# Performance work log

Measured on AMD Instinct MI355X. Metric: run time of the kernel, lower is better.

Reference implementation:

```python
import jax, jax.numpy as jnp
import numpy as np

D = 1024
H = 16
HD = D // H
EPS = 1e-5

def _layernorm(x, g, b):
    xf = x.astype(jnp.float32)
    mu = jnp.mean(xf, axis=-1, keepdims=True)
    var = jnp.mean(jnp.square(xf - mu), axis=-1, keepdims=True)
    return ((xf - mu) * jax.lax.rsqrt(var + EPS) * g + b).astype(x.dtype)

def setup_inputs() -> dict:
    key = jax.random.key(0)
    ks = jax.random.split(key, 12)
    B, S = 4, 1024
    s_in = 1.0 / np.sqrt(D)
    inp = {
        "x": jax.random.normal(ks[0], (B, S, D), dtype=jnp.float32),
        "in_proj_w": jax.random.normal(ks[1], (3 * D, D), dtype=jnp.float32) * s_in,
        "in_proj_b": jnp.zeros((3 * D,), dtype=jnp.float32),
        "out_w": jax.random.normal(ks[2], (D, D), dtype=jnp.float32) * s_in,
        "out_b": jnp.zeros((D,), dtype=jnp.float32),
        "ln1_g": jnp.ones((D,), dtype=jnp.float32),
        "ln1_b": jnp.zeros((D,), dtype=jnp.float32),
        "fc_w": jax.random.normal(ks[3], (4 * D, D), dtype=jnp.float32) * s_in,
        "fc_b": jnp.zeros((4 * D,), dtype=jnp.float32),
        "proj_w": jax.random.normal(ks[4], (D, 4 * D), dtype=jnp.float32) * (1.0 / np.sqrt(4 * D)),
        "proj_b": jnp.zeros((D,), dtype=jnp.float32),
        "ln2_g": jnp.ones((D,), dtype=jnp.float32),
        "ln2_b": jnp.zeros((D,), dtype=jnp.float32),
    }
    return inp

def reference(x, in_proj_w, in_proj_b, out_w, out_b, ln1_g, ln1_b,
              fc_w, fc_b, proj_w, proj_b, ln2_g, ln2_b):
    B, S, _ = x.shape
    scaling = float(HD) ** -0.5
    # --- attention sublayer ---
    h = _layernorm(x, ln1_g, ln1_b)
    qkv = h @ in_proj_w.T + in_proj_b              # [B,S,3D]
    q, k, v = jnp.split(qkv, 3, axis=-1)
    q = (q * scaling).reshape(B, S, H, HD).transpose(0, 2, 1, 3)  # [B,H,S,hd]
    k = k.reshape(B, S, H, HD).transpose(0, 2, 1, 3)
    v = v.reshape(B, S, H, HD).transpose(0, 2, 1, 3)
    attn = jax.nn.softmax(jnp.einsum('bhqd,bhkd->bhqk', q, k), axis=-1)
    o = jnp.einsum('bhqk,bhkd->bhqd', attn, v).transpose(0, 2, 1, 3).reshape(B, S, D)
    x = x + o @ out_w.T + out_b
    # --- MLP sublayer (QuickGELU) ---
    h = _layernorm(x, ln2_g, ln2_b)
    u = h @ fc_w.T + fc_b                          # [B,S,4D]
    u = u * jax.nn.sigmoid(1.702 * u)
    x = x + u @ proj_w.T + proj_b
    return x
```

## Files before the change

### kernel.cpp

```cpp
#include <hip/hip_runtime.h>
#include <math.h>

#define D_MODEL 1024
#define SEQ     1024
#define BATCH   4
#define NTOK    (BATCH * SEQ)

typedef __bf16 bf16;
using bfrag = __attribute__((ext_vector_type(8))) __bf16;
using ffrag = __attribute__((ext_vector_type(4))) float;

__device__ __forceinline__ ffrag mfma16(bfrag a, bfrag b, ffrag c) {
  return __builtin_amdgcn_mfma_f32_16x16x32_bf16(a, b, c, 0, 0, 0);
}

__device__ __forceinline__ void gload_lds16(const void* g, void* l) {
  __builtin_amdgcn_global_load_lds(
      (const __attribute__((address_space(1))) void*)g,
      (__attribute__((address_space(3))) void*)l, 16, 0, 0);
}

__global__ void convert_all(const float* __restrict__ s0, bf16* __restrict__ d0, int n0,
                            const float* __restrict__ s1, bf16* __restrict__ d1, int n1,
                            const float* __restrict__ s2, bf16* __restrict__ d2, int n2,
                            const float* __restrict__ s3, bf16* __restrict__ d3, int n3,
                            float scale, int limit0) {
  const float* src; bf16* dst; int n; int limit = 0;
  switch (blockIdx.y) {
    case 0: src = s0; dst = d0; n = n0; limit = limit0; break;
    case 1: src = s1; dst = d1; n = n1; break;
    case 2: src = s2; dst = d2; n = n2; break;
    default: src = s3; dst = d3; n = n3; break;
  }
  int i = blockIdx.x * blockDim.x + threadIdx.x;
  const int stride = gridDim.x * blockDim.x;
  for (; i < n; i += stride) {
    float4 v = ((const float4*)src)[i];
    float sc = (i < limit) ? scale : 1.0f;
    bf16* d = dst + (size_t)i * 4;
    d[0] = (bf16)(v.x * sc); d[1] = (bf16)(v.y * sc);
    d[2] = (bf16)(v.z * sc); d[3] = (bf16)(v.w * sc);
  }
}

__global__ void scale_bias(const float* __restrict__ src, float* __restrict__ dst,
                           int n, int limit, float scale) {
  int i = blockIdx.x * blockDim.x + threadIdx.x;
  if (i < n) dst[i] = src[i] * (i < limit ? scale : 1.0f);
}

__global__ __launch_bounds__(256) void ln_row(const float* __restrict__ x,
                                              const float* __restrict__ gamma,
                                              const float* __restrict__ beta,
                                              bf16* __restrict__ out) {
  const int row = blockIdx.x, tid = threadIdx.x;
  const float4 v = ((const float4*)(x + (size_t)row * D_MODEL))[tid];
  float s  = v.x + v.y + v.z + v.w;
  float ss = v.x * v.x + v.y * v.y + v.z * v.z + v.w * v.w;
#pragma unroll
  for (int off = 32; off >= 1; off >>= 1) {
    s  += __shfl_xor(s, off);
    ss += __shfl_xor(ss, off);
  }
  __shared__ float rs[4], rss[4];
  const int w = tid >> 6;
  if ((tid & 63) == 0) { rs[w] = s; rss[w] = ss; }
  __syncthreads();
  s  = rs[0] + rs[1] + rs[2] + rs[3];
  ss = rss[0] + rss[1] + rss[2] + rss[3];
  const float mu   = s * (1.0f / D_MODEL);
  const float var  = ss * (1.0f / D_MODEL) - mu * mu;
  const float rstd = rsqrtf(var + 1e-5f);
  const float4 gv = ((const float4*)gamma)[tid];
  const float4 bv = ((const float4*)beta)[tid];
  bf16* o = out + (size_t)row * D_MODEL + tid * 4;
  o[0] = (bf16)((v.x - mu) * rstd * gv.x + bv.x);
  o[1] = (bf16)((v.y - mu) * rstd * gv.y + bv.y);
  o[2] = (bf16)((v.z - mu) * rstd * gv.z + bv.z);
  o[3] = (bf16)((v.w - mu) * rstd * gv.w + bv.w);
}

template <int EPI>
__global__ __launch_bounds__(256, 2) void gemm_bt(
    const bf16* __restrict__ A, const bf16* __restrict__ B,
    const float* __restrict__ bias, const float* __restrict__ resid,
    float* __restrict__ outF, bf16* __restrict__ outB,
    int M, int N, int K) {
  __shared__ bf16 As[2][128 * 32];
  __shared__ bf16 Bs[2][128 * 32];
  const int tid = threadIdx.x;
  const int lane = tid & 63, w = tid >> 6;
  const int wm = w >> 1, wn = w & 1;
  const int ql = lane & 15, lg = lane >> 4;
  const int m0 = blockIdx.x * 128, n0 = blockIdx.y * 128;

  ffrag acc[4][4];
#pragma unroll
  for (int i = 0; i < 4; i++)
#pragma unroll
    for (int j = 0; j < 4; j++) acc[i][j] = ffrag{0.f, 0.f, 0.f, 0.f};

  const int r0 = tid >> 2;
  const int jsw = (tid & 3) ^ (r0 & 3);
  const bf16* a0 = A + (size_t)(m0 + r0) * K + jsw * 8;
  const bf16* a1 = A + (size_t)(m0 + 64 + r0) * K + jsw * 8;
  const bf16* b0 = B + (size_t)(n0 + r0) * K + jsw * 8;
  const bf16* b1 = B + (size_t)(n0 + 64 + r0) * K + jsw * 8;
  const int lo = w * 512;

  auto STAGE = [&](int bs, int kk) {
    gload_lds16(a0 + kk, &As[bs][lo]);
    gload_lds16(a1 + kk, &As[bs][2048 + lo]);
    gload_lds16(b0 + kk, &Bs[bs][lo]);
    gload_lds16(b1 + kk, &Bs[bs][2048 + lo]);
  };

  STAGE(0, 0);
  __syncthreads();

  int cur = 0;
  for (int k0 = 0; k0 < K; k0 += 32) {
    if (k0 + 32 < K) STAGE(cur ^ 1, k0 + 32);
    bfrag af[4], bfr[4];
#pragma unroll
    for (int i = 0; i < 4; i++) {
      const int row = wm * 64 + i * 16 + ql;
      af[i] = *(const bfrag*)&As[cur][row * 32 + ((lg ^ (row & 3)) * 8)];
    }
#pragma unroll
    for (int j = 0; j < 4; j++) {
      const int row = wn * 64 + j * 16 + ql;
      bfr[j] = *(const bfrag*)&Bs[cur][row * 32 + ((lg ^ (row & 3)) * 8)];
    }
#pragma unroll
    for (int i = 0; i < 4; i++)
#pragma unroll
      for (int j = 0; j < 4; j++)
        acc[i][j] = mfma16(af[i], bfr[j], acc[i][j]);
    __syncthreads();
    cur ^= 1;
  }

#pragma unroll
  for (int i = 0; i < 4; i++) {
    const int row = m0 + wm * 64 + i * 16 + lg * 4;
#pragma unroll
    for (int j = 0; j < 4; j++) {
      const int col = n0 + wn * 64 + j * 16 + ql;
      const float bv = bias[col];
#pragma unroll
      for (int r = 0; r < 4; r++) {
        float v = acc[i][j][r] + bv;
        const size_t idx = (size_t)(row + r) * N + col;
        if (EPI == 0) {
          outB[idx] = (bf16)v;
        } else if (EPI == 1) {
          outF[idx] = v + resid[idx];
        } else {
          outB[idx] = (bf16)(v / (1.0f + __expf(-1.702f * v)));
        }
      }
    }
  }
}

template <int EPI>
__global__ __launch_bounds__(256, 4) void gemm_bt64(
    const bf16* __restrict__ A, const bf16* __restrict__ B,
    const float* __restrict__ bias, const float* __restrict__ resid,
    float* __restrict__ outF, bf16* __restrict__ outB,
    int M, int N, int K) {
  __shared__ bf16 As[2][64 * 64];
  __shared__ bf16 Bs[2][64 * 64];
  const int tid = threadIdx.x;
  const int lane = tid & 63, w = tid >> 6;
  const int wm = w >> 1, wn = w & 1;
  const int ql = lane & 15, lg = lane >> 4;
  const int m0 = blockIdx.x * 64, n0 = blockIdx.y * 64;

  ffrag acc[2][2];
#pragma unroll
  for (int i = 0; i < 2; i++)
#pragma unroll
    for (int j = 0; j < 2; j++) acc[i][j] = ffrag{0.f, 0.f, 0.f, 0.f};

  const int r0 = tid >> 3;
  const int jsw = ((tid & 7) ^ (r0 & 7)) * 8;
  const bf16* a0 = A + (size_t)(m0 + r0) * K + jsw;
  const bf16* a1 = A + (size_t)(m0 + 32 + r0) * K + jsw;
  const bf16* b0 = B + (size_t)(n0 + r0) * K + jsw;
  const bf16* b1 = B + (size_t)(n0 + 32 + r0) * K + jsw;
  const int lo = tid * 8;

  auto STAGE = [&](int bs, int kk) {
    gload_lds16(a0 + kk, &As[bs][lo]);
    gload_lds16(a1 + kk, &As[bs][2048 + lo]);
    gload_lds16(b0 + kk, &Bs[bs][lo]);
    gload_lds16(b1 + kk, &Bs[bs][2048 + lo]);
  };

  STAGE(0, 0);
  __syncthreads();

  int cur = 0;
  for (int k0 = 0; k0 < K; k0 += 64) {
    if (k0 + 64 < K) STAGE(cur ^ 1, k0 + 64);
    bfrag af[2][2], bfr[2][2];
#pragma unroll
    for (int i = 0; i < 2; i++) {
      const int row = wm * 32 + i * 16 + ql;
      const int r7 = row & 7;
#pragma unroll
      for (int kc = 0; kc < 2; kc++)
        af[i][kc] = *(const bfrag*)&As[cur][row * 64 + (((lg + 4 * kc) ^ r7) * 8)];
    }
#pragma unroll
    for (int j = 0; j < 2; j++) {
      const int row = wn * 32 + j * 16 + ql;
      const int r7 = row & 7;
#pragma unroll
      for (int kc = 0; kc < 2; kc++)
        bfr[j][kc] = *(const bfrag*)&Bs[cur][row * 64 + (((lg + 4 * kc) ^ r7) * 8)];
    }
#pragma unroll
    for (int kc = 0; kc < 2; kc++)
#pragma unroll
      for (int i = 0; i < 2; i++)
#pragma unroll
        for (int j = 0; j < 2; j++)
          acc[i][j] = mfma16(af[i][kc], bfr[j][kc], acc[i][j]);
    __syncthreads();
    cur ^= 1;
  }

#pragma unroll
  for (int i = 0; i < 2; i++) {
    const int row = m0 + wm * 32 + i * 16 + lg * 4;
#pragma unroll
    for (int j = 0; j < 2; j++) {
      const int col = n0 + wn * 32 + j * 16 + ql;
      const float bv = bias[col];
#pragma unroll
      for (int r = 0; r < 4; r++) {
        float v = acc[i][j][r] + bv;
        const size_t idx = (size_t)(row + r) * N + col;
        if (EPI == 0) {
          outB[idx] = (bf16)v;
        } else if (EPI == 1) {
          outF[idx] = v + resid[idx];
        } else {
          outB[idx] = (bf16)(v / (1.0f + __expf(-1.702f * v)));
        }
      }
    }
  }
}

__global__ __launch_bounds__(256) void transpose_v(const bf16* __restrict__ qkv,
                                                   bf16* __restrict__ vt) {
  __shared__ bf16 T[64 * 66];
  const int tid = threadIdx.x;
  const int bh = blockIdx.y, b = bh >> 4, h = bh & 15;
  const int s0 = blockIdx.x * 64;
  const bf16* src = qkv + (size_t)b * SEQ * 3072 + 2048 + h * 64;

  const int sl = tid >> 3, c = tid & 7;
#pragma unroll
  for (int p = 0; p < 2; p++) {
    const int s = sl + p * 32;
    const bfrag v = *(const bfrag*)(src + (size_t)(s0 + s) * 3072 + c * 8);
#pragma unroll
    for (int e = 0; e < 8; e++) T[s * 66 + c * 8 + e] = v[e];
  }
  __syncthreads();
  bf16* dst = vt + (size_t)bh * 64 * 1024;
#pragma unroll
  for (int p = 0; p < 2; p++) {
    const int d = sl + p * 32;
    bfrag o;
#pragma unroll
    for (int e = 0; e < 8; e++) o[e] = T[(c * 8 + e) * 66 + d];
    *(bfrag*)(dst + (size_t)d * 1024 + s0 + c * 8) = o;
  }
}

__global__ __launch_bounds__(256, 3) void flash_attn(const bf16* __restrict__ qkv,
                                                     const bf16* __restrict__ vt,
                                                     bf16* __restrict__ o) {
  __shared__ bf16 Kl[128 * 64];
  __shared__ bf16 Vl[64 * 128];
  __shared__ bf16 Pl[4 * 16 * 136];
  const int tid = threadIdx.x, lane = tid & 63, wid = tid >> 6;
  const int ql = lane & 15, lg = lane >> 4;
  const int bh = blockIdx.y, b = bh >> 4, h = bh & 15;
  const int qrow0 = blockIdx.x * 64 + wid * 16;
  const size_t headq = (size_t)b * SEQ * 3072 + (size_t)h * 64;

  const bf16* qp = qkv + headq + (size_t)(qrow0 + ql) * 3072 + lg * 8;
  const bfrag q0 = *(const bfrag*)qp;
  const bfrag q1 = *(const bfrag*)(qp + 32);

  float mrun[4], lrun[4];
  ffrag oacc[4];
#pragma unroll
  for (int r = 0; r < 4; r++) { mrun[r] = -1e30f; lrun[r] = 0.0f; }
#pragma unroll
  for (int f = 0; f < 4; f++) oacc[f] = ffrag{0.f, 0.f, 0.f, 0.f};

  const int kr0 = tid >> 3;
  const int kjsw = ((tid & 7) ^ (kr0 & 7)) * 8;
  const bf16* kp = qkv + headq + 1024 + (size_t)kr0 * 3072 + kjsw;
  const int vr_ = tid >> 4, vlc = tid & 15;
  const bf16* vhead = vt + (size_t)bh * 64 * 1024;
  bf16* Pw = Pl + wid * 2176;

  for (int kt = 0; kt < SEQ; kt += 128) {
#pragma unroll
    for (int pp = 0; pp < 4; pp++)
      gload_lds16(kp + (size_t)(kt + pp * 32) * 3072, &Kl[pp * 2048 + tid * 8]);
#pragma unroll
    for (int pp = 0; pp < 4; pp++) {
      const int vr = pp * 16 + vr_;
      const int gc = vlc ^ (vr & 7);
      gload_lds16(vhead + (size_t)vr * 1024 + kt + gc * 8, &Vl[(pp * 256 + tid) * 8]);
    }
    __syncthreads();

    ffrag sa[8];
    __builtin_amdgcn_s_setprio(1);
#pragma unroll
    for (int sub = 0; sub < 8; sub++) {
      const int krow = sub * 16 + ql;
      const int r7 = krow & 7;
      const bfrag kf0 = *(const bfrag*)&Kl[krow * 64 + ((lg ^ r7) * 8)];
      const bfrag kf1 = *(const bfrag*)&Kl[krow * 64 + (((lg + 4) ^ r7) * 8)];
      ffrag s4 = ffrag{0.f, 0.f, 0.f, 0.f};
      s4 = mfma16(q0, kf0, s4);
      s4 = mfma16(q1, kf1, s4);
      sa[sub] = s4;
    }
    __builtin_amdgcn_s_setprio(0);

    float lmax[4];
#pragma unroll
    for (int r = 0; r < 4; r++) {
      float m = sa[0][r];
#pragma unroll
      for (int sub = 1; sub < 8; sub++) m = fmaxf(m, sa[sub][r]);
      lmax[r] = m;
    }
    bool ok = (lmax[0] - mrun[0] <= 8.0f) && (lmax[1] - mrun[1] <= 8.0f) &&
              (lmax[2] - mrun[2] <= 8.0f) && (lmax[3] - mrun[3] <= 8.0f);
    if (!__all(ok)) {
#pragma unroll
      for (int r = 0; r < 4; r++) {
        float mx = lmax[r];
        mx = fmaxf(mx, __shfl_xor(mx, 1));
        mx = fmaxf(mx, __shfl_xor(mx, 2));
        mx = fmaxf(mx, __shfl_xor(mx, 4));
        mx = fmaxf(mx, __shfl_xor(mx, 8));
        const float mnew = fmaxf(mrun[r], mx);
        const float corr = exp2f(mrun[r] - mnew);
        lrun[r] *= corr;
#pragma unroll
        for (int f = 0; f < 4; f++) oacc[f][r] *= corr;
        mrun[r] = mnew;
      }
    }
#pragma unroll
    for (int r = 0; r < 4; r++) {
      float pv[8], srow = 0.f;
#pragma unroll
      for (int sub = 0; sub < 8; sub++) {
        pv[sub] = exp2f(sa[sub][r] - mrun[r]);
        srow += pv[sub];
      }
      srow += __shfl_xor(srow, 1);
      srow += __shfl_xor(srow, 2);
      srow += __shfl_xor(srow, 4);
      srow += __shfl_xor(srow, 8);
      lrun[r] += srow;
      bf16* prow = Pw + (lg * 4 + r) * 136;
#pragma unroll
      for (int sub = 0; sub < 8; sub++) prow[sub * 16 + ql] = (bf16)pv[sub];
    }

    bfrag pa[4];
#pragma unroll
    for (int kc = 0; kc < 4; kc++)
      pa[kc] = *(const bfrag*)&Pw[ql * 136 + kc * 32 + lg * 8];
    __builtin_amdgcn_s_setprio(1);
#pragma unroll
    for (int f = 0; f < 4; f++) {
      const int vrow = f * 16 + ql;
      const int r7 = vrow & 7;
#pragma unroll
      for (int kc = 0; kc < 4; kc++) {
        const bfrag vf = *(const bfrag*)&Vl[vrow * 128 + (((kc * 4 + lg) ^ r7) * 8)];
        oacc[f] = mfma16(pa[kc], vf, oacc[f]);
      }
    }
    __builtin_amdgcn_s_setprio(0);
    __syncthreads();
  }

#pragma unroll
  for (int f = 0; f < 4; f++) {
#pragma unroll
    for (int r = 0; r < 4; r++) {
      const size_t orow = (size_t)b * SEQ + qrow0 + lg * 4 + r;
      o[orow * 1024 + h * 64 + f * 16 + ql] = (bf16)(oacc[f][r] / lrun[r]);
    }
  }
}

extern "C" void kernel_launch(void* const* d_in, const int* in_sizes, int n_in,
                              void* d_out, int out_size, void* d_ws, size_t ws_size,
                              hipStream_t stream) {
  (void)in_sizes; (void)n_in; (void)out_size; (void)ws_size;
  const float* x      = (const float*)d_in[0];
  const float* in_w   = (const float*)d_in[1];
  const float* in_b   = (const float*)d_in[2];
  const float* out_w  = (const float*)d_in[3];
  const float* out_b  = (const float*)d_in[4];
  const float* ln1_g  = (const float*)d_in[5];
  const float* ln1_b  = (const float*)d_in[6];
  const float* fc_w   = (const float*)d_in[7];
  const float* fc_b   = (const float*)d_in[8];
  const float* proj_w = (const float*)d_in[9];
  const float* proj_b = (const float*)d_in[10];
  const float* ln2_g  = (const float*)d_in[11];
  const float* ln2_b  = (const float*)d_in[12];
  float* out = (float*)d_out;

  char* p = (char*)d_ws;
  auto alloc = [&](size_t bytes) { char* r = p; p += (bytes + 255) & ~255ull; return r; };
  bf16* w_qkv  = (bf16*)alloc((size_t)3072 * 1024 * 2);
  bf16* w_out  = (bf16*)alloc((size_t)1024 * 1024 * 2);
  bf16* w_fc   = (bf16*)alloc((size_t)4096 * 1024 * 2);
  bf16* w_proj = (bf16*)alloc((size_t)1024 * 4096 * 2);
  float* b_qkv = (float*)alloc((size_t)3072 * 4);
  bf16* hbuf   = (bf16*)alloc((size_t)NTOK * 1024 * 2);
  float* x2    = (float*)alloc((size_t)NTOK * 1024 * 4);
  bf16* qkv    = (bf16*)alloc((size_t)NTOK * 3072 * 2);
  bf16* aout   = (bf16*)alloc((size_t)NTOK * 1024 * 2);
  bf16* ubuf   = qkv;
  bf16* vtb    = (bf16*)x2;

  const float scaling = 0.125f * 1.44269504089f;
  convert_all<<<dim3(1024, 4), 256, 0, stream>>>(
      in_w, w_qkv, 3072 * 1024 / 4,
      out_w, w_out, 1024 * 1024 / 4,
      fc_w, w_fc, 4096 * 1024 / 4,
      proj_w, w_proj, 4096 * 1024 / 4,
      scaling, 1024 * 1024 / 4);
  scale_bias<<<12, 256, 0, stream>>>(in_b, b_qkv, 3072, 1024, scaling);

  ln_row<<<NTOK, 256, 0, stream>>>(x, ln1_g, ln1_b, hbuf);
  gemm_bt<0><<<dim3(32, 24), 256, 0, stream>>>(hbuf, w_qkv, b_qkv, nullptr,
                                               nullptr, qkv, NTOK, 3072, 1024);
  transpose_v<<<dim3(16, 64), 256, 0, stream>>>(qkv, vtb);
  flash_attn<<<dim3(16, 64), 256, 0, stream>>>(qkv, vtb, aout);
  gemm_bt64<1><<<dim3(64, 16), 256, 0, stream>>>(aout, w_out, out_b, x,
                                                 x2, nullptr, NTOK, 1024, 1024);
  ln_row<<<NTOK, 256, 0, stream>>>(x2, ln2_g, ln2_b, hbuf);
  gemm_bt<2><<<dim3(32, 32), 256, 0, stream>>>(hbuf, w_fc, fc_b, nullptr,
                                               nullptr, ubuf, NTOK, 4096, 1024);
  gemm_bt64<1><<<dim3(64, 16), 256, 0, stream>>>(ubuf, w_proj, proj_b, x2,
                                                 out, nullptr, NTOK, 1024, 4096);
}
```

Baseline: 233.9 us.

## Triple-buffer gemm_bt with single barrier, drop gemm_bt64, defer flash row-sum reduction

The 128x128 GEMM moves from a double-buffered LDS pipeline to a three-stage ring. Two tiles are prefetched ahead, and explicit vmcnt waits plus one barrier per k-step replace the two __syncthreads. The 64x64 GEMM is removed, so both output-projection GEMMs now use the 128x128 kernel with only 256 blocks, which risks underfilling the GPU. Flash attention accumulates per-lane partial row sums and does the cross-lane shuffle reduction once at the end instead of every tile, then multiplies by a reciprocal.

```diff
diff --git a/kernel.cpp b/kernel.cpp
--- a/kernel.cpp
+++ b/kernel.cpp
@@ -86,8 +86,8 @@
     const float* __restrict__ bias, const float* __restrict__ resid,
     float* __restrict__ outF, bf16* __restrict__ outB,
     int M, int N, int K) {
-  __shared__ bf16 As[2][128 * 32];
-  __shared__ bf16 Bs[2][128 * 32];
+  __shared__ bf16 As[3][128 * 32];
+  __shared__ bf16 Bs[3][128 * 32];
   const int tid = threadIdx.x;
   const int lane = tid & 63, w = tid >> 6;
   const int wm = w >> 1, wn = w & 1;
@@ -116,11 +116,20 @@
   };
 
   STAGE(0, 0);
-  __syncthreads();
+  STAGE(1, 32);
 
   int cur = 0;
   for (int k0 = 0; k0 < K; k0 += 32) {
-    if (k0 + 32 < K) STAGE(cur ^ 1, k0 + 32);
+    if (k0 + 32 < K) {
+      asm volatile("s_waitcnt vmcnt(4) lgkmcnt(0)" ::: "memory");
+    } else {
+      asm volatile("s_waitcnt vmcnt(0) lgkmcnt(0)" ::: "memory");
+    }
+    __builtin_amdgcn_s_barrier();
+    if (k0 + 64 < K) {
+      int nb = cur + 2; if (nb >= 3) nb -= 3;
+      STAGE(nb, k0 + 64);
+    }
     bfrag af[4], bfr[4];
 #pragma unroll
     for (int i = 0; i < 4; i++) {
@@ -137,9 +146,9 @@
 #pragma unroll
       for (int j = 0; j < 4; j++)
         acc[i][j] = mfma16(af[i], bfr[j], acc[i][j]);
-    __syncthreads();
-    cur ^= 1;
-  }
+    cur = (cur + 1 == 3) ? 0 : (cur + 1);
+  }
+  asm volatile("" ::: "memory");
 
 #pragma unroll
   for (int i = 0; i < 4; i++) {
@@ -164,98 +173,6 @@
   }
 }
 
-template <int EPI>
-__global__ __launch_bounds__(256, 4) void gemm_bt64(
-    const bf16* __restrict__ A, const bf16* __restrict__ B,
-    const float* __restrict__ bias, const float* __restrict__ resid,
-    float* __restrict__ outF, bf16* __restrict__ outB,
-    int M, int N, int K) {
-  __shared__ bf16 As[2][64 * 64];
-  __shared__ bf16 Bs[2][64 * 64];
-  const int tid = threadIdx.x;
-  const int lane = tid & 63, w = tid >> 6;
-  const int wm = w >> 1, wn = w & 1;
-  const int ql = lane & 15, lg = lane >> 4;
-  const int m0 = blockIdx.x * 64, n0 = blockIdx.y * 64;
-
-  ffrag acc[2][2];
-#pragma unroll
-  for (int i = 0; i < 2; i++)
-#pragma unroll
-    for (int j = 0; j < 2; j++) acc[i][j] = ffrag{0.f, 0.f, 0.f, 0.f};
-
-  const int r0 = tid >> 3;
-  const int jsw = ((tid & 7) ^ (r0 & 7)) * 8;
-  const bf16* a0 = A + (size_t)(m0 + r0) * K + jsw;
-  const bf16* a1 = A + (size_t)(m0 + 32 + r0) * K + jsw;
-  const bf16* b0 = B + (size_t)(n0 + r0) * K + jsw;
-  const bf16* b1 = B + (size_t)(n0 + 32 + r0) * K + jsw;
-  const int lo = tid * 8;
-
-  auto STAGE = [&](int bs, int kk) {
-    gload_lds16(a0 + kk, &As[bs][lo]);
-    gload_lds16(a1 + kk, &As[bs][2048 + lo]);
-    gload_lds16(b0 + kk, &Bs[bs][lo]);
-    gload_lds16(b1 + kk, &Bs[bs][2048 + lo]);
-  };
-
-  STAGE(0, 0);
-  __syncthreads();
-
-  int cur = 0;
-  for (int k0 = 0; k0 < K; k0 += 64) {
-    if (k0 + 64 < K) STAGE(cur ^ 1, k0 + 64);
-    bfrag af[2][2], bfr[2][2];
-#pragma unroll
-    for (int i = 0; i < 2; i++) {
-      const int row = wm * 32 + i * 16 + ql;
-      const int r7 = row & 7;
-#pragma unroll
-      for (int kc = 0; kc < 2; kc++)
-        af[i][kc] = *(const bfrag*)&As[cur][row * 64 + (((lg + 4 * kc) ^ r7) * 8)];
-    }
-#pragma unroll
-    for (int j = 0; j < 2; j++) {
-      const int row = wn * 32 + j * 16 + ql;
-      const int r7 = row & 7;
-#pragma unroll
-      for (int kc = 0; kc < 2; kc++)
-        bfr[j][kc] = *(const bfrag*)&Bs[cur][row * 64 + (((lg + 4 * kc) ^ r7) * 8)];
-    }
-#pragma unroll
-    for (int kc = 0; kc < 2; kc++)
-#pragma unroll
-      for (int i = 0; i < 2; i++)
-#pragma unroll
-        for (int j = 0; j < 2; j++)
-          acc[i][j] = mfma16(af[i][kc], bfr[j][kc], acc[i][j]);
-    __syncthreads();
-    cur ^= 1;
-  }
-
-#pragma unroll
-  for (int i = 0; i < 2; i++) {
-    const int row = m0 + wm * 32 + i * 16 + lg * 4;
-#pragma unroll
-    for (int j = 0; j < 2; j++) {
-      const int col = n0 + wn * 32 + j * 16 + ql;
-      const float bv = bias[col];
-#pragma unroll
-      for (int r = 0; r < 4; r++) {
-        float v = acc[i][j][r] + bv;
-        const size_t idx = (size_t)(row + r) * N + col;
-        if (EPI == 0) {
-          outB[idx] = (bf16)v;
-        } else if (EPI == 1) {
-          outF[idx] = v + resid[idx];
-        } else {
-          outB[idx] = (bf16)(v / (1.0f + __expf(-1.702f * v)));
-        }
-      }
-    }
-  }
-}
-
 __global__ __launch_bounds__(256) void transpose_v(const bf16* __restrict__ qkv,
                                                    bf16* __restrict__ vt) {
   __shared__ bf16 T[64 * 66];
@@ -369,20 +286,15 @@
     }
 #pragma unroll
     for (int r = 0; r < 4; r++) {
-      float pv[8], srow = 0.f;
+      float srow = 0.f;
+      bf16* prow = Pw + (lg * 4 + r) * 136;
 #pragma unroll
       for (int sub = 0; sub < 8; sub++) {
-        pv[sub] = exp2f(sa[sub][r] - mrun[r]);
-        srow += pv[sub];
+        const float pv = exp2f(sa[sub][r] - mrun[r]);
+        srow += pv;
+        prow[sub * 16 + ql] = (bf16)pv;
       }
-      srow += __shfl_xor(srow, 1);
-      srow += __shfl_xor(srow, 2);
-      srow += __shfl_xor(srow, 4);
-      srow += __shfl_xor(srow, 8);
       lrun[r] += srow;
-      bf16* prow = Pw + (lg * 4 + r) * 136;
-#pragma unroll
-      for (int sub = 0; sub < 8; sub++) prow[sub * 16 + ql] = (bf16)pv[sub];
     }
 
     bfrag pa[4];
@@ -404,12 +316,22 @@
     __syncthreads();
   }
 
+  float rinv[4];
+#pragma unroll
+  for (int r = 0; r < 4; r++) {
+    float ls = lrun[r];
+    ls += __shfl_xor(ls, 1);
+    ls += __shfl_xor(ls, 2);
+    ls += __shfl_xor(ls, 4);
+    ls += __shfl_xor(ls, 8);
+    rinv[r] = 1.0f / ls;
+  }
 #pragma unroll
   for (int f = 0; f < 4; f++) {
 #pragma unroll
     for (int r = 0; r < 4; r++) {
       const size_t orow = (size_t)b * SEQ + qrow0 + lg * 4 + r;
-      o[orow * 1024 + h * 64 + f * 16 + ql] = (bf16)(oacc[f][r] / lrun[r]);
+      o[orow * 1024 + h * 64 + f * 16 + ql] = (bf16)(oacc[f][r] * rinv[r]);
     }
   }
 }
@@ -461,11 +383,11 @@
                                                nullptr, qkv, NTOK, 3072, 1024);
   transpose_v<<<dim3(16, 64), 256, 0, stream>>>(qkv, vtb);
   flash_attn<<<dim3(16, 64), 256, 0, stream>>>(qkv, vtb, aout);
-  gemm_bt64<1><<<dim3(64, 16), 256, 0, stream>>>(aout, w_out, out_b, x,
-                                                 x2, nullptr, NTOK, 1024, 1024);
+  gemm_bt<1><<<dim3(32, 8), 256, 0, stream>>>(aout, w_out, out_b, x,
+                                              x2, nullptr, NTOK, 1024, 1024);
   ln_row<<<NTOK, 256, 0, stream>>>(x2, ln2_g, ln2_b, hbuf);
   gemm_bt<2><<<dim3(32, 32), 256, 0, stream>>>(hbuf, w_fc, fc_b, nullptr,
                                                nullptr, ubuf, NTOK, 4096, 1024);
-  gemm_bt64<1><<<dim3(64, 16), 256, 0, stream>>>(ubuf, w_proj, proj_b, x2,
-                                                 out, nullptr, NTOK, 1024, 4096);
-}
+  gemm_bt<1><<<dim3(32, 8), 256, 0, stream>>>(ubuf, w_proj, proj_b, x2,
+                                              out, nullptr, NTOK, 1024, 4096);
+}
```

After: 276.1 us. 18.0% more time.
